# Kernel tuning notes

Hardware: AMD Instinct MI355X
Metric: run time of the kernel (lower is better)

The kernel has to match this reference:

```python
import jax, jax.numpy as jnp
import numpy as np

K_SIZES = (3, 9)          # per-level local window sizes (both < 13)
K_NUM = tuple((k * k - 1) // 2 for k in K_SIZES)  # topk sizes: (4, 40)
BN_EPS = 1e-5


def _make_local_ids(W, patch_id, k):
    """Replicates get_local_index (k<13 branch): wrap-around kxk window minus center."""
    r = k // 2
    out = []
    for i in patch_id:
        i = int(i)
        ix, iy = i // W, i % W
        wx = np.zeros(W)
        wy = np.zeros(W)
        for j in range(-r, r + 1):
            wx[(ix + j) % W] = 1.0
            wy[(iy + j) % W] = 1.0
        wgt = (wy[None, :] * wx[:, None]).reshape(-1)  # row-major: idx = x*W + y
        wgt[i] = 0.0
        out.append(np.nonzero(wgt)[0])
    return np.stack(out).astype(np.int64)  # [N, k*k-1]


def setup_inputs() -> dict:
    key = jax.random.key(0)
    ks = jax.random.split(key, 8)
    B = 8
    feat0 = jax.random.normal(ks[0], (B, 512, 8, 8), jnp.float32)
    feat1 = jax.random.normal(ks[1], (B, 64, 128, 128), jnp.float32)
    rng = np.random.default_rng(0)
    patch_id0 = rng.permutation(8 * 8)[:64]
    patch_id1 = rng.permutation(128 * 128)[:512]
    local_id0 = _make_local_ids(8, patch_id0, K_SIZES[0])    # [64, 8]
    local_id1 = _make_local_ids(128, patch_id1, K_SIZES[1])  # [512, 80]
    s = 0.02
    return dict(
        feat0=feat0, feat1=feat1,
        W1=jax.random.normal(ks[2], (1024, 512), jnp.float32) * s,
        b1=jnp.zeros((1024,), jnp.float32),
        gamma=jnp.ones((1024,), jnp.float32),
        beta=jnp.zeros((1024,), jnp.float32),
        W2=jax.random.normal(ks[3], (256, 1024), jnp.float32) * s,
        b2=jnp.zeros((256,), jnp.float32),
        W3=jax.random.normal(ks[4], (256, 64), jnp.float32) * s,
        b3=jnp.zeros((256,), jnp.float32),
        W4=jax.random.normal(ks[5], (256, 256), jnp.float32) * s,
        b4=jnp.zeros((256,), jnp.float32),
        patch_id0=jnp.asarray(patch_id0, jnp.int64 if jax.config.jax_enable_x64 else jnp.int32),
        patch_id1=jnp.asarray(patch_id1, jnp.int64 if jax.config.jax_enable_x64 else jnp.int32),
        local_id0=jnp.asarray(local_id0, jnp.int64 if jax.config.jax_enable_x64 else jnp.int32),
        local_id1=jnp.asarray(local_id1, jnp.int64 if jax.config.jax_enable_x64 else jnp.int32),
        patch_size=128,
    )


def _sample(feat, patch_id, local_id, k_num):
    """gather local patches -> cosine sim vs center -> topk -> gather winners."""
    B, C, H, W = feat.shape
    fr = jnp.transpose(feat, (0, 2, 3, 1)).reshape(B, H * W, C)  # [B, HW, C]
    norm = jnp.linalg.norm(fr, axis=-1, keepdims=True)
    xn = fr / jnp.maximum(norm, 1e-12)                 # F.normalize(dim=-1)
    loc = xn[:, local_id]                              # [B, N, L, C]
    cen = xn[:, patch_id]                              # [B, N, C]
    sim = jnp.einsum('bnlc,bnc->bnl', loc, cen)        # [B, N, L]
    _, top = jax.lax.top_k(sim, k_num)                 # [B, N, k]
    N, L = local_id.shape
    top = top.reshape(B * N, k_num, 1)
    x_loc = fr[:, local_id].reshape(B * N, L, C)
    x_loc = jnp.take_along_axis(x_loc, jnp.broadcast_to(top, (B * N, k_num, C)), axis=1)
    x_cen = fr[:, patch_id].reshape(B * N, 1, C)
    return jnp.concatenate([x_cen, x_loc], axis=1)     # [B*N, 1+k, C]


def reference(feat0, feat1, W1, b1, gamma, beta, W2, b2, W3, b3, W4, b4,
              patch_id0, patch_id1, local_id0, local_id1, patch_size):
    # level 0: h == patch_size // 16 -> adaptive_avg_pool over (1+k) axis, then mlp1
    x0 = _sample(feat0, patch_id0, local_id0, K_NUM[0])  # [B*N0, 1+k0, 512]
    x0 = x0.mean(axis=1)                                 # adaptive_avg_pool2d -> (1, dim)
    h = x0 @ W1.T + b1
    mu = h.mean(axis=0)
    var = h.var(axis=0)                                  # BatchNorm1d (training stats)
    h = (h - mu) / jnp.sqrt(var + BN_EPS) * gamma + beta
    out0 = jax.nn.relu(h) @ W2.T + b2                    # [B*N0, 256]

    # level 1: h == patch_size -> mlp2 per (center+neighbors) row, then l2norm
    x1 = _sample(feat1, patch_id1, local_id1, K_NUM[1])  # [B*N1, 1+k1, 64]
    BN1, M, C1 = x1.shape
    y = x1.reshape(-1, C1)
    y = jax.nn.relu(y @ W3.T + b3) @ W4.T + b4           # [B*N1*(1+k1), 256]
    y = y / (jnp.linalg.norm(y, axis=1, keepdims=True) + 1e-7)  # Normalize(2)
    out1 = y.reshape(BN1, M, -1)                         # [B*N1, 1+k1, 256]
    return out0, out1
```

## Files before the change

### kernel.cpp

```cpp
#include <hip/hip_runtime.h>
#include <math.h>

typedef _Float16 f16x8 __attribute__((ext_vector_type(8)));
typedef float f32x4 __attribute__((ext_vector_type(4)));


__global__ __launch_bounds__(256) void k_wprep(
    const float* __restrict__ W3, const float* __restrict__ W4,
    unsigned short* __restrict__ PB3h, unsigned short* __restrict__ PB3l,
    unsigned short* __restrict__ PB4h, unsigned short* __restrict__ PB4l)
{
    const int e = blockIdx.x * 256 + threadIdx.x;
    if (e < 16384) {
        const int j = e & 7, l = (e >> 3) & 63, ks = (e >> 9) & 1, nt = e >> 10;
        const int n = nt * 16 + (l & 15);
        const int k = ks * 32 + (l >> 4) * 8 + j;
        const float w = W3[n * 64 + k];
        const _Float16 hi = (_Float16)w;
        const _Float16 lo = (_Float16)(w - (float)hi);
        ((_Float16*)PB3h)[e] = hi;
        ((_Float16*)PB3l)[e] = lo;
    }
    {
        const int j = e & 7, l = (e >> 3) & 63, ks = (e >> 9) & 7, nt = e >> 12;
        const int n = nt * 16 + (l & 15);
        const int k = ks * 32 + (l >> 4) * 8 + j;
        const float w = W4[n * 256 + k];
        const _Float16 hi = (_Float16)w;
        const _Float16 lo = (_Float16)(w - (float)hi);
        ((_Float16*)PB4h)[e] = hi;
        ((_Float16*)PB4l)[e] = lo;
    }
}

__global__ __launch_bounds__(256) void k_transpose1(
    const float* __restrict__ feat1, float* __restrict__ featT)
{
    __shared__ float tile[64][65];
    const int b = blockIdx.y;
    const int p0 = blockIdx.x * 64;
    const int tid = threadIdx.x;
    const float* fb = feat1 + (size_t)b * 64 * 16384;
    float* ft = featT + (size_t)b * 16384 * 64;
    #pragma unroll
    for (int it = 0; it < 16; ++it) {
        const int e = it * 256 + tid;
        const int c = e >> 6, p = e & 63;
        tile[p][c] = fb[(size_t)c * 16384 + p0 + p];
    }
    __syncthreads();
    #pragma unroll
    for (int it = 0; it < 16; ++it) {
        const int e = it * 256 + tid;
        const int p = e >> 6, c = e & 63;
        ft[(size_t)(p0 + p) * 64 + c] = tile[p][c];
    }
}

__global__ __launch_bounds__(256) void k_zero(unsigned* __restrict__ p, int n)
{
    const int i = blockIdx.x * 256 + threadIdx.x;
    if (i < n) p[i] = 0u;
}

__global__ __launch_bounds__(128) void k_sims1T(
    const float* __restrict__ featT, const int* __restrict__ patch_id1,
    const int* __restrict__ local_id1, int* __restrict__ idx,
    unsigned* __restrict__ cnt)
{
    __shared__ float cen[64];
    __shared__ double sims[80];
    __shared__ double cnorm;

    const int row = blockIdx.x;
    const int b = row >> 9;
    const int n = row & 511;
    const int tid = threadIdx.x;
    const float* ft = featT + (size_t)b * 16384 * 64;
    const int pid = patch_id1[n];
    const int* lids = local_id1 + n * 80;

    if (tid < 64) cen[tid] = ft[(size_t)pid * 64 + tid];
    __syncthreads();

    if (tid < 64) {
        double v = (double)cen[tid];
        double s = v * v;
        for (int o = 32; o > 0; o >>= 1) s += __shfl_down(s, o);
        if (tid == 0) { s = sqrt(s); cnorm = (s < 1e-12) ? 1e-12 : s; }
    }
    __syncthreads();

    if (tid < 80) {
        const float4* rp = (const float4*)(ft + (size_t)lids[tid] * 64);
        double d = 0.0, q = 0.0;
        #pragma unroll
        for (int k = 0; k < 16; ++k) {
            const float4 v4 = rp[k];
            double v;
            v = (double)v4.x; d += v * (double)cen[4*k+0]; q += v*v;
            v = (double)v4.y; d += v * (double)cen[4*k+1]; q += v*v;
            v = (double)v4.z; d += v * (double)cen[4*k+2]; q += v*v;
            v = (double)v4.w; d += v * (double)cen[4*k+3]; q += v*v;
        }
        double nl = sqrt(q); if (nl < 1e-12) nl = 1e-12;
        sims[tid] = d / (nl * cnorm);
    }
    __syncthreads();

    if (tid < 80) {
        const double s = sims[tid];
        int rank = 0;
        for (int j = 0; j < 80; ++j) {
            const double sj = sims[j];
            rank += (sj > s) || (sj == s && j < tid);
        }
        if (rank < 40) {
            idx[row * 41 + 1 + rank] = lids[tid];
            atomicAdd(&cnt[b * 16384 + lids[tid]], 1u);
        }
    }
    if (tid == 0) {
        idx[row * 41] = pid;
        atomicAdd(&cnt[b * 16384 + pid], 1u);
    }
}

__global__ __launch_bounds__(256) void k_scan(
    const unsigned* __restrict__ cnt, unsigned* __restrict__ off,
    unsigned* __restrict__ cursor)
{
    __shared__ unsigned ssum[256];
    const int img = blockIdx.x;
    const int t = threadIdx.x;
    const unsigned* c = cnt + img * 16384;
    unsigned s = 0;
    for (int i = 0; i < 64; ++i) s += c[t * 64 + i];
    ssum[t] = s;
    __syncthreads();
    if (t == 0) {
        unsigned run = 0;
        for (int i = 0; i < 256; ++i) { const unsigned v = ssum[i]; ssum[i] = run; run += v; }
    }
    __syncthreads();
    unsigned run = ssum[t];
    unsigned* o  = off + img * 16384;
    unsigned* cu = cursor + img * 16384;
    for (int i = 0; i < 64; ++i) {
        const int p = t * 64 + i;
        o[p] = run; cu[p] = run;
        run += c[p];
    }
}

__global__ __launch_bounds__(256) void k_fill(
    const int* __restrict__ idx, unsigned* __restrict__ cursor,
    int* __restrict__ slots)
{
    const int e = blockIdx.x * 256 + threadIdx.x;
    if (e >= 4096 * 41) return;
    const int row = e / 41;
    const int img = row >> 9;
    const int pix = idx[e];
    const unsigned pos = atomicAdd(&cursor[img * 16384 + pix], 1u);
    slots[img * 20992 + pos] = e;
}

__global__ __launch_bounds__(256, 4) void k_mlp_fused(
    const float* __restrict__ featb,
    const unsigned short* __restrict__ PB3h, const unsigned short* __restrict__ PB3l,
    const unsigned short* __restrict__ PB4h, const unsigned short* __restrict__ PB4l,
    const float* __restrict__ b3, const float* __restrict__ b4,
    const unsigned* __restrict__ cnt, const unsigned* __restrict__ off,
    const int* __restrict__ slots, float* __restrict__ out1)
{
    __shared__ __align__(16) unsigned char smem[33792];
    _Float16 (*XH)[72]  = (_Float16(*)[72])smem;
    _Float16 (*XL)[72]  = (_Float16(*)[72])(smem + 4608);
    _Float16 (*TH)[264] = (_Float16(*)[264])smem;
    _Float16 (*TL)[264] = (_Float16(*)[264])(smem + 16896);
    __shared__ float rsums[2][2][16];

    const int tid = threadIdx.x;
    const int blk = blockIdx.x;
    const int img = blk >> 9;
    const int p0 = (blk & 511) * 32;
    const float* fb = featb + (size_t)img * 64 * 16384;

    {
        const int p = tid & 31;
        const int cg = tid >> 5;
        #pragma unroll
        for (int k = 0; k < 8; ++k) {
            const int c = cg * 8 + k;
            const float v = fb[(size_t)c * 16384 + p0 + p];
            const _Float16 hi = (_Float16)v;
            XH[p][c] = hi;
            XL[p][c] = (_Float16)(v - (float)hi);
        }
    }
    __syncthreads();

    const int lane = tid & 63;
    const int w = tid >> 6;
    const int mt = w & 1;
    const int nh = w >> 1;
    const int lrow = lane & 15;
    const int kblk = lane >> 4;

    f16x8 ah[2], al[2];
    #pragma unroll
    for (int ks = 0; ks < 2; ++ks) {
        ah[ks] = *(const f16x8*)&XH[mt*16 + lrow][ks*32 + kblk*8];
        al[ks] = *(const f16x8*)&XL[mt*16 + lrow][ks*32 + kblk*8];
    }
    __syncthreads();

    {
        const f16x8* B3H = (const f16x8*)PB3h;
        const f16x8* B3L = (const f16x8*)PB3l;
        #pragma unroll
        for (int t = 0; t < 8; ++t) {
            const int nt = nh*8 + t;
            const f16x8 bh0 = B3H[(nt*2 + 0)*64 + lane];
            const f16x8 bl0 = B3L[(nt*2 + 0)*64 + lane];
            const f16x8 bh1 = B3H[(nt*2 + 1)*64 + lane];
            const f16x8 bl1 = B3L[(nt*2 + 1)*64 + lane];
            f32x4 acc = {0.f, 0.f, 0.f, 0.f};
            acc = __builtin_amdgcn_mfma_f32_16x16x32_f16(al[0], bh0, acc, 0, 0, 0);
            acc = __builtin_amdgcn_mfma_f32_16x16x32_f16(ah[0], bl0, acc, 0, 0, 0);
            acc = __builtin_amdgcn_mfma_f32_16x16x32_f16(ah[0], bh0, acc, 0, 0, 0);
            acc = __builtin_amdgcn_mfma_f32_16x16x32_f16(al[1], bh1, acc, 0, 0, 0);
            acc = __builtin_amdgcn_mfma_f32_16x16x32_f16(ah[1], bl1, acc, 0, 0, 0);
            acc = __builtin_amdgcn_mfma_f32_16x16x32_f16(ah[1], bh1, acc, 0, 0, 0);
            const float bias = b3[nt*16 + lrow];
            #pragma unroll
            for (int r = 0; r < 4; ++r) {
                const float tv = fmaxf(acc[r] + bias, 0.f);
                const _Float16 hi = (_Float16)tv;
                TH[mt*16 + kblk*4 + r][nt*16 + lrow] = hi;
                TL[mt*16 + kblk*4 + r][nt*16 + lrow] = (_Float16)(tv - (float)hi);
            }
        }
    }
    __syncthreads();

    f32x4 acc2[8];
    #pragma unroll
    for (int t = 0; t < 8; ++t) acc2[t] = (f32x4){0.f, 0.f, 0.f, 0.f};
    {
        const f16x8* B4H = (const f16x8*)PB4h;
        const f16x8* B4L = (const f16x8*)PB4l;
        #pragma unroll 2
        for (int ks = 0; ks < 8; ++ks) {
            const f16x8 a2h = *(const f16x8*)&TH[mt*16 + lrow][ks*32 + kblk*8];
            const f16x8 a2l = *(const f16x8*)&TL[mt*16 + lrow][ks*32 + kblk*8];
            #pragma unroll
            for (int th = 0; th < 2; ++th) {
                f16x8 bh[4], bl[4];
                #pragma unroll
                for (int q = 0; q < 4; ++q) {
                    const int nt = nh*8 + th*4 + q;
                    bh[q] = B4H[(nt*8 + ks)*64 + lane];
                    bl[q] = B4L[(nt*8 + ks)*64 + lane];
                }
                #pragma unroll
                for (int q = 0; q < 4; ++q) {
                    const int t = th*4 + q;
                    acc2[t] = __builtin_amdgcn_mfma_f32_16x16x32_f16(a2l, bh[q], acc2[t], 0, 0, 0);
                    acc2[t] = __builtin_amdgcn_mfma_f32_16x16x32_f16(a2h, bl[q], acc2[t], 0, 0, 0);
                    acc2[t] = __builtin_amdgcn_mfma_f32_16x16x32_f16(a2h, bh[q], acc2[t], 0, 0, 0);
                }
            }
        }
    }

    float p[4] = {0.f, 0.f, 0.f, 0.f};
    #pragma unroll
    for (int t = 0; t < 8; ++t) {
        const float bias = b4[(nh*8 + t)*16 + lrow];
        #pragma unroll
        for (int r = 0; r < 4; ++r) {
            acc2[t][r] += bias;
            p[r] += acc2[t][r] * acc2[t][r];
        }
    }
    #pragma unroll
    for (int r = 0; r < 4; ++r)
        for (int o = 1; o < 16; o <<= 1) p[r] += __shfl_xor(p[r], o);
    if (lrow == 0) {
        #pragma unroll
        for (int r = 0; r < 4; ++r) rsums[mt][nh][kblk*4 + r] = p[r];
    }
    __syncthreads();
    float inv[4];
    #pragma unroll
    for (int r = 0; r < 4; ++r) {
        const float s = rsums[mt][0][kblk*4 + r] + rsums[mt][1][kblk*4 + r];
        inv[r] = 1.f / (sqrtf(s) + 1e-7f);
    }

    const unsigned* cntp = cnt + img * 16384;
    const unsigned* offp = off + img * 16384;
    const int* slotp = slots + img * 20992;
    #pragma unroll
    for (int r = 0; r < 4; ++r) {
        const int row = mt*16 + kblk*4 + r;
        const int pix = p0 + row;
        const unsigned deg = cntp[pix];
        const unsigned st = offp[pix];
        float y[8];
        #pragma unroll
        for (int t = 0; t < 8; ++t) y[t] = acc2[t][r] * inv[r];
        for (unsigned s = 0; s < deg; ++s) {
            const int e = slotp[st + s];
            float* dst = out1 + (size_t)e * 256 + nh*128 + lrow;
            #pragma unroll
            for (int t = 0; t < 8; ++t) dst[t*16] = y[t];
        }
    }
}

__global__ __launch_bounds__(128) void k_sims1(
    const float* __restrict__ feat1, const int* __restrict__ patch_id1,
    const int* __restrict__ local_id1, int* __restrict__ idx)
{
    __shared__ float cen[64];
    __shared__ double sims[80];
    __shared__ double cnorm;

    const int row = blockIdx.x;
    const int b = row >> 9;
    const int n = row & 511;
    const int tid = threadIdx.x;
    const float* fb = feat1 + (size_t)b * 64 * 16384;
    const int pid = patch_id1[n];
    const int* lids = local_id1 + n * 80;

    if (tid < 64) cen[tid] = fb[(size_t)tid * 16384 + pid];
    __syncthreads();

    if (tid < 64) {
        double v = (double)cen[tid];
        double s = v * v;
        for (int o = 32; o > 0; o >>= 1) s += __shfl_down(s, o);
        if (tid == 0) { s = sqrt(s); cnorm = (s < 1e-12) ? 1e-12 : s; }
    }
    __syncthreads();

    if (tid < 80) {
        const int lpix = lids[tid];
        double d = 0.0, q = 0.0;
        for (int c = 0; c < 64; ++c) {
            double v = (double)fb[(size_t)c * 16384 + lpix];
            d += v * (double)cen[c];
            q += v * v;
        }
        double nl = sqrt(q); if (nl < 1e-12) nl = 1e-12;
        sims[tid] = d / (nl * cnorm);
    }
    __syncthreads();

    if (tid < 80) {
        const double s = sims[tid];
        int rank = 0;
        for (int j = 0; j < 80; ++j) {
            const double sj = sims[j];
            rank += (sj > s) || (sj == s && j < tid);
        }
        if (rank < 40) idx[row * 41 + 1 + rank] = lids[tid];
    }
    if (tid == 0) idx[row * 41] = pid;
}

__global__ __launch_bounds__(256) void k_mlp_pix2(
    const float* __restrict__ featb,
    const float* __restrict__ W3T, const float* __restrict__ b3,
    const float* __restrict__ W4T, const float* __restrict__ b4,
    float* __restrict__ ybuf, int ybufStride)
{
    __shared__ __align__(16) float xs[32 * 68];
    __shared__ __align__(16) float t1s[32 * 256];

    const int tid = threadIdx.x;
    const int blk = blockIdx.x;
    const int img = blk >> 9;
    const int p0 = (blk & 511) * 32;
    const float* fb = featb + (size_t)img * 64 * 16384;
    float* yb = ybuf + (size_t)img * (size_t)ybufStride;

    {
        const int p = tid & 31;
        const int cg = tid >> 5;
        #pragma unroll
        for (int k = 0; k < 8; ++k) {
            const int c = cg * 8 + k;
            xs[p * 68 + c] = fb[(size_t)c * 16384 + p0 + p];
        }
    }
    __syncthreads();

    const int jg = tid & 63;
    const int g = tid >> 6;
    const int j0 = jg * 4;
    const int mb = g * 8;

    {
        float acc[8][4];
        #pragma unroll
        for (int r = 0; r < 8; ++r) {
            acc[r][0] = 0.f; acc[r][1] = 0.f; acc[r][2] = 0.f; acc[r][3] = 0.f;
        }
        const float4* Wf = (const float4*)W3T;
        const float4* xsf = (const float4*)xs;
        #pragma unroll 4
        for (int cq = 0; cq < 16; ++cq) {
            const float4 wA = Wf[(cq * 4 + 0) * 64 + jg];
            const float4 wB = Wf[(cq * 4 + 1) * 64 + jg];
            const float4 wC = Wf[(cq * 4 + 2) * 64 + jg];
            const float4 wD = Wf[(cq * 4 + 3) * 64 + jg];
            #pragma unroll
            for (int r = 0; r < 8; ++r) {
                const float4 x4 = xsf[(mb + r) * 17 + cq];
                acc[r][0] += x4.x*wA.x + x4.y*wB.x + x4.z*wC.x + x4.w*wD.x;
                acc[r][1] += x4.x*wA.y + x4.y*wB.y + x4.z*wC.y + x4.w*wD.y;
                acc[r][2] += x4.x*wA.z + x4.y*wB.z + x4.z*wC.z + x4.w*wD.z;
                acc[r][3] += x4.x*wA.w + x4.y*wB.w + x4.z*wC.w + x4.w*wD.w;
            }
        }
        const float bb0 = b3[j0], bb1 = b3[j0+1], bb2 = b3[j0+2], bb3 = b3[j0+3];
        #pragma unroll
        for (int r = 0; r < 8; ++r) {
            float4 o4;
            o4.x = fmaxf(acc[r][0] + bb0, 0.f);
            o4.y = fmaxf(acc[r][1] + bb1, 0.f);
            o4.z = fmaxf(acc[r][2] + bb2, 0.f);
            o4.w = fmaxf(acc[r][3] + bb3, 0.f);
            *(float4*)&t1s[(mb + r) * 256 + j0] = o4;
        }
    }
    __syncthreads();

    {
        float acc[8][4];
        #pragma unroll
        for (int r = 0; r < 8; ++r) {
            acc[r][0] = 0.f; acc[r][1] = 0.f; acc[r][2] = 0.f; acc[r][3] = 0.f;
        }
        const float4* Wf = (const float4*)W4T;
        const float4* t1f = (const float4*)t1s;
        #pragma unroll 2
        for (int kq = 0; kq < 64; ++kq) {
            const float4 wA = Wf[(kq * 4 + 0) * 64 + jg];
            const float4 wB = Wf[(kq * 4 + 1) * 64 + jg];
            const float4 wC = Wf[(kq * 4 + 2) * 64 + jg];
            const float4 wD = Wf[(kq * 4 + 3) * 64 + jg];
            #pragma unroll
            for (int r = 0; r < 8; ++r) {
                const float4 t4 = t1f[(mb + r) * 64 + kq];
                acc[r][0] += t4.x*wA.x + t4.y*wB.x + t4.z*wC.x + t4.w*wD.x;
                acc[r][1] += t4.x*wA.y + t4.y*wB.y + t4.z*wC.y + t4.w*wD.y;
                acc[r][2] += t4.x*wA.z + t4.y*wB.z + t4.z*wC.z + t4.w*wD.z;
                acc[r][3] += t4.x*wA.w + t4.y*wB.w + t4.z*wC.w + t4.w*wD.w;
            }
        }
        const float bb0 = b4[j0], bb1 = b4[j0+1], bb2 = b4[j0+2], bb3 = b4[j0+3];
        #pragma unroll
        for (int r = 0; r < 8; ++r) {
            const float y0 = acc[r][0] + bb0;
            const float y1 = acc[r][1] + bb1;
            const float y2 = acc[r][2] + bb2;
            const float y3 = acc[r][3] + bb3;
            float p = y0*y0 + y1*y1 + y2*y2 + y3*y3;
            for (int o = 1; o < 64; o <<= 1) p += __shfl_xor(p, o);
            const float inv = 1.f / (sqrtf(p) + 1e-7f);
            float4 o4 = make_float4(y0*inv, y1*inv, y2*inv, y3*inv);
            *(float4*)&yb[(size_t)(p0 + mb + r) * 256 + j0] = o4;
        }
    }
}

__global__ __launch_bounds__(256) void k_wtrans(
    const float* __restrict__ W3, const float* __restrict__ W4,
    float* __restrict__ W3T, float* __restrict__ W4T)
{
    const int t = threadIdx.x;
    const int j = blockIdx.x;
    W4T[(size_t)t * 256 + j] = W4[(size_t)j * 256 + t];
    if (j < 64) W3T[(size_t)j * 256 + t] = W3[(size_t)t * 64 + j];
}

__global__ __launch_bounds__(256) void k_gather1(
    const float* __restrict__ ybuf, int ybufStride,
    const int* __restrict__ idxb, float* __restrict__ out1b)
{
    __shared__ int pix[41];
    const int bn = blockIdx.x;
    const int img = bn >> 9;
    const int tid = threadIdx.x;
    if (tid < 41) pix[tid] = idxb[bn * 41 + tid];
    __syncthreads();
    const float4* yb4 = (const float4*)(ybuf + (size_t)img * (size_t)ybufStride);
    float4* o4 = (float4*)(out1b + (size_t)bn * 41 * 256);
    for (int e = tid; e < 41 * 64; e += 256) {
        const int mi = e >> 6, j4 = e & 63;
        o4[mi * 64 + j4] = yb4[pix[mi] * 64 + j4];
    }
}

__global__ __launch_bounds__(256) void k_branch1(
    const float* __restrict__ feat1, const int* __restrict__ patch_id1,
    const int* __restrict__ local_id1, const float* __restrict__ W3,
    const float* __restrict__ b3, const float* __restrict__ W4,
    const float* __restrict__ b4, float* __restrict__ out1)
{
    __shared__ __align__(16) float xs[44 * 64];
    __shared__ __align__(16) float t1s[44 * 256];
    __shared__ double sims[80];
    __shared__ int winners[40];
    __shared__ float cen[64];
    __shared__ double cnorm;

    const int row = blockIdx.x;
    const int b = row >> 9;
    const int n = row & 511;
    const int tid = threadIdx.x;
    const float* fb = feat1 + (size_t)b * 64 * 16384;
    const int pid = patch_id1[n];
    const int* lids = local_id1 + n * 80;

    if (tid < 64) cen[tid] = fb[(size_t)tid * 16384 + pid];
    __syncthreads();

    if (tid < 64) {
        double v = (double)cen[tid];
        double s = v * v;
        for (int o = 32; o > 0; o >>= 1) s += __shfl_down(s, o);
        if (tid == 0) { s = sqrt(s); cnorm = (s < 1e-12) ? 1e-12 : s; }
    }
    __syncthreads();

    if (tid < 80) {
        const int lpix = lids[tid];
        double d = 0.0, q = 0.0;
        for (int c = 0; c < 64; ++c) {
            double v = (double)fb[(size_t)c * 16384 + lpix];
            d += v * (double)cen[c];
            q += v * v;
        }
        double nl = sqrt(q); if (nl < 1e-12) nl = 1e-12;
        sims[tid] = d / (nl * cnorm);
    }
    __syncthreads();

    if (tid < 80) {
        const double s = sims[tid];
        int rank = 0;
        for (int j = 0; j < 80; ++j) {
            const double sj = sims[j];
            rank += (sj > s) || (sj == s && j < tid);
        }
        if (rank < 40) winners[rank] = tid;
    }
    __syncthreads();

    for (int m = tid; m < 44 * 64; m += 256) {
        const int mi = m >> 6, c = m & 63;
        float v;
        if (mi >= 1 && mi <= 40) v = fb[(size_t)c * 16384 + lids[winners[mi - 1]]];
        else v = cen[c];
        xs[m] = v;
    }
    __syncthreads();

    const int jg = tid & 63;
    const int g = tid >> 6;
    const int j0 = jg * 4;
    const int mb = g * 11;

    {
        float acc[11][4];
        #pragma unroll
        for (int r = 0; r < 11; ++r) {
            acc[r][0] = 0.f; acc[r][1] = 0.f; acc[r][2] = 0.f; acc[r][3] = 0.f;
        }
        const float4* W3f = (const float4*)W3;
        const float4* xsf = (const float4*)xs;
        #pragma unroll 4
        for (int c4 = 0; c4 < 16; ++c4) {
            const float4 w0 = W3f[(j0 + 0) * 16 + c4];
            const float4 w1 = W3f[(j0 + 1) * 16 + c4];
            const float4 w2 = W3f[(j0 + 2) * 16 + c4];
            const float4 w3 = W3f[(j0 + 3) * 16 + c4];
            #pragma unroll
            for (int r = 0; r < 11; ++r) {
                const float4 x4 = xsf[(mb + r) * 16 + c4];
                acc[r][0] += x4.x*w0.x + x4.y*w0.y + x4.z*w0.z + x4.w*w0.w;
                acc[r][1] += x4.x*w1.x + x4.y*w1.y + x4.z*w1.z + x4.w*w1.w;
                acc[r][2] += x4.x*w2.x + x4.y*w2.y + x4.z*w2.z + x4.w*w2.w;
                acc[r][3] += x4.x*w3.x + x4.y*w3.y + x4.z*w3.z + x4.w*w3.w;
            }
        }
        const float bb0 = b3[j0], bb1 = b3[j0+1], bb2 = b3[j0+2], bb3 = b3[j0+3];
        #pragma unroll
        for (int r = 0; r < 11; ++r) {
            float4 o4;
            o4.x = fmaxf(acc[r][0] + bb0, 0.f);
            o4.y = fmaxf(acc[r][1] + bb1, 0.f);
            o4.z = fmaxf(acc[r][2] + bb2, 0.f);
            o4.w = fmaxf(acc[r][3] + bb3, 0.f);
            *(float4*)&t1s[(mb + r) * 256 + j0] = o4;
        }
    }
    __syncthreads();

    {
        float acc[11][4];
        #pragma unroll
        for (int r = 0; r < 11; ++r) {
            acc[r][0] = 0.f; acc[r][1] = 0.f; acc[r][2] = 0.f; acc[r][3] = 0.f;
        }
        const float4* W4f = (const float4*)W4;
        const float4* t1f = (const float4*)t1s;
        #pragma unroll 2
        for (int j4 = 0; j4 < 64; ++j4) {
            const float4 w0 = W4f[(j0 + 0) * 64 + j4];
            const float4 w1 = W4f[(j0 + 1) * 64 + j4];
            const float4 w2 = W4f[(j0 + 2) * 64 + j4];
            const float4 w3 = W4f[(j0 + 3) * 64 + j4];
            #pragma unroll
            for (int r = 0; r < 11; ++r) {
                const float4 t4 = t1f[(mb + r) * 64 + j4];
                acc[r][0] += t4.x*w0.x + t4.y*w0.y + t4.z*w0.z + t4.w*w0.w;
                acc[r][1] += t4.x*w1.x + t4.y*w1.y + t4.z*w1.z + t4.w*w1.w;
                acc[r][2] += t4.x*w2.x + t4.y*w2.y + t4.z*w2.z + t4.w*w2.w;
                acc[r][3] += t4.x*w3.x + t4.y*w3.y + t4.z*w3.z + t4.w*w3.w;
            }
        }
        const float bb0 = b4[j0], bb1 = b4[j0+1], bb2 = b4[j0+2], bb3 = b4[j0+3];
        #pragma unroll
        for (int r = 0; r < 11; ++r) {
            const float y0 = acc[r][0] + bb0;
            const float y1 = acc[r][1] + bb1;
            const float y2 = acc[r][2] + bb2;
            const float y3 = acc[r][3] + bb3;
            float p = y0*y0 + y1*y1 + y2*y2 + y3*y3;
            for (int o = 1; o < 64; o <<= 1) p += __shfl_xor(p, o);
            const float inv = 1.f / (sqrtf(p) + 1e-7f);
            const int mi = mb + r;
            if (mi < 41) {
                float4 o4 = make_float4(y0*inv, y1*inv, y2*inv, y3*inv);
                *(float4*)&out1[((size_t)row * 41 + mi) * 256 + j0] = o4;
            }
        }
    }
}

__global__ __launch_bounds__(64) void k_sample0(
    const float* __restrict__ feat0, const int* __restrict__ patch_id0,
    const int* __restrict__ local_id0, float* __restrict__ x0m)
{
    __shared__ float cen[512];
    __shared__ float loc[8][512];
    __shared__ double sims[8];
    __shared__ int winners[4];
    __shared__ double cnorm;

    const int row = blockIdx.x;
    const int b = row >> 6;
    const int n = row & 63;
    const int t = threadIdx.x;
    const float* fb = feat0 + (size_t)b * 512 * 64;
    const int pid = patch_id0[n];

    for (int c = t; c < 512; c += 64) cen[c] = fb[(size_t)c * 64 + pid];
    for (int l = 0; l < 8; ++l) {
        const int lp = local_id0[n * 8 + l];
        for (int c = t; c < 512; c += 64) loc[l][c] = fb[(size_t)c * 64 + lp];
    }
    __syncthreads();

    double cs = 0.0;
    for (int c = t; c < 512; c += 64) { double v = (double)cen[c]; cs += v * v; }
    for (int o = 32; o > 0; o >>= 1) cs += __shfl_down(cs, o);
    if (t == 0) { cs = sqrt(cs); cnorm = (cs < 1e-12) ? 1e-12 : cs; }
    __syncthreads();

    for (int l = 0; l < 8; ++l) {
        double d = 0.0, q = 0.0;
        for (int c = t; c < 512; c += 64) {
            double v = (double)loc[l][c];
            d += v * (double)cen[c];
            q += v * v;
        }
        for (int o = 32; o > 0; o >>= 1) { d += __shfl_down(d, o); q += __shfl_down(q, o); }
        if (t == 0) {
            double nl = sqrt(q); if (nl < 1e-12) nl = 1e-12;
            sims[l] = d / (nl * cnorm);
        }
    }
    __syncthreads();

    if (t < 8) {
        const double s = sims[t];
        int rank = 0;
        for (int j = 0; j < 8; ++j) {
            const double sj = sims[j];
            rank += (sj > s) || (sj == s && j < t);
        }
        if (rank < 4) winners[rank] = t;
    }
    __syncthreads();

    for (int c = t; c < 512; c += 64) {
        float a = cen[c];
        for (int r = 0; r < 4; ++r) a += loc[winners[r]][c];
        x0m[(size_t)row * 512 + c] = a * 0.2f;
    }
}

__global__ __launch_bounds__(128) void k_gemm1(
    const float* __restrict__ x, const float* __restrict__ W1,
    const float* __restrict__ b1, float* __restrict__ h)
{
    __shared__ __align__(16) float xsr[8 * 512];
    const int i0 = blockIdx.y * 8;
    const int tid = threadIdx.x;
    const int j0 = blockIdx.x * 512 + tid * 4;

    const float4* xg = (const float4*)(x + (size_t)i0 * 512);
    float4* xl = (float4*)xsr;
    #pragma unroll
    for (int e = 0; e < 8; ++e) xl[e * 128 + tid] = xg[e * 128 + tid];
    __syncthreads();

    float acc[8][4];
    #pragma unroll
    for (int r = 0; r < 8; ++r) {
        acc[r][0] = 0.f; acc[r][1] = 0.f; acc[r][2] = 0.f; acc[r][3] = 0.f;
    }
    const float4* W1f = (const float4*)W1;
    const float4* xf  = (const float4*)xsr;
    #pragma unroll 4
    for (int c4 = 0; c4 < 128; ++c4) {
        const float4 w0 = W1f[(size_t)(j0 + 0) * 128 + c4];
        const float4 w1 = W1f[(size_t)(j0 + 1) * 128 + c4];
        const float4 w2 = W1f[(size_t)(j0 + 2) * 128 + c4];
        const float4 w3 = W1f[(size_t)(j0 + 3) * 128 + c4];
        #pragma unroll
        for (int r = 0; r < 8; ++r) {
            const float4 x4 = xf[r * 128 + c4];
            acc[r][0] += x4.x*w0.x + x4.y*w0.y + x4.z*w0.z + x4.w*w0.w;
            acc[r][1] += x4.x*w1.x + x4.y*w1.y + x4.z*w1.z + x4.w*w1.w;
            acc[r][2] += x4.x*w2.x + x4.y*w2.y + x4.z*w2.z + x4.w*w2.w;
            acc[r][3] += x4.x*w3.x + x4.y*w3.y + x4.z*w3.z + x4.w*w3.w;
        }
    }
    const float bb0 = b1[j0], bb1 = b1[j0+1], bb2 = b1[j0+2], bb3 = b1[j0+3];
    #pragma unroll
    for (int r = 0; r < 8; ++r) {
        float4 o4 = make_float4(acc[r][0] + bb0, acc[r][1] + bb1,
                                acc[r][2] + bb2, acc[r][3] + bb3);
        *(float4*)&h[(size_t)(i0 + r) * 1024 + j0] = o4;
    }
}

__global__ __launch_bounds__(64) void k_bnstats(
    const float* __restrict__ h, float* __restrict__ mu, float* __restrict__ rstd)
{
    const int j = blockIdx.x;
    const int t = threadIdx.x;
    float s = 0.f, ss = 0.f;
    for (int i = t; i < 512; i += 64) {
        const float v = h[(size_t)i * 1024 + j];
        s += v; ss += v * v;
    }
    for (int o = 32; o > 0; o >>= 1) { s += __shfl_down(s, o); ss += __shfl_down(ss, o); }
    if (t == 0) {
        const float m = s * (1.f / 512.f);
        const float var = ss * (1.f / 512.f) - m * m;
        mu[j] = m;
        rstd[j] = rsqrtf(var + 1e-5f);
    }
}

__global__ __launch_bounds__(256) void k_bnapply(
    float* __restrict__ h, const float* __restrict__ mu, const float* __restrict__ rstd,
    const float* __restrict__ gamma, const float* __restrict__ beta)
{
    const int e = blockIdx.x * 256 + threadIdx.x;
    const int jb = (e & 255) * 4;
    float4 v = ((float4*)h)[e];
    v.x = fmaxf((v.x - mu[jb+0]) * rstd[jb+0] * gamma[jb+0] + beta[jb+0], 0.f);
    v.y = fmaxf((v.y - mu[jb+1]) * rstd[jb+1] * gamma[jb+1] + beta[jb+1], 0.f);
    v.z = fmaxf((v.z - mu[jb+2]) * rstd[jb+2] * gamma[jb+2] + beta[jb+2], 0.f);
    v.w = fmaxf((v.w - mu[jb+3]) * rstd[jb+3] * gamma[jb+3] + beta[jb+3], 0.f);
    ((float4*)h)[e] = v;
}

__global__ __launch_bounds__(256) void k_gemm2(
    const float* __restrict__ h, const float* __restrict__ W2,
    const float* __restrict__ b2, float* __restrict__ out0)
{
    __shared__ __align__(16) float hs[8 * 1024];
    const int i0 = blockIdx.x * 8;
    const int j = threadIdx.x;

    const float4* hg = (const float4*)(h + (size_t)i0 * 1024);
    float4* hl = (float4*)hs;
    #pragma unroll
    for (int e = 0; e < 8; ++e) hl[e * 256 + j] = hg[e * 256 + j];
    __syncthreads();

    float acc[8];
    #pragma unroll
    for (int r = 0; r < 8; ++r) acc[r] = 0.f;
    const float4* wr = (const float4*)(W2 + (size_t)j * 1024);
    const float4* hf = (const float4*)hs;
    #pragma unroll 4
    for (int k4 = 0; k4 < 256; ++k4) {
        const float4 w = wr[k4];
        #pragma unroll
        for (int r = 0; r < 8; ++r) {
            const float4 a = hf[r * 256 + k4];
            acc[r] += a.x*w.x + a.y*w.y + a.z*w.z + a.w*w.w;
        }
    }
    const float bb = b2[j];
    #pragma unroll
    for (int r = 0; r < 8; ++r)
        out0[(size_t)(i0 + r) * 256 + j] = acc[r] + bb;
}

extern "C" void kernel_launch(void* const* d_in, const int* in_sizes, int n_in,
                              void* d_out, int out_size, void* d_ws, size_t ws_size,
                              hipStream_t stream) {
    const float* feat0 = (const float*)d_in[0];
    const float* feat1 = (const float*)d_in[1];
    const float* W1    = (const float*)d_in[2];
    const float* b1    = (const float*)d_in[3];
    const float* gamma = (const float*)d_in[4];
    const float* beta  = (const float*)d_in[5];
    const float* W2    = (const float*)d_in[6];
    const float* b2    = (const float*)d_in[7];
    const float* W3    = (const float*)d_in[8];
    const float* b3    = (const float*)d_in[9];
    const float* W4    = (const float*)d_in[10];
    const float* b4    = (const float*)d_in[11];
    const int* patch_id0 = (const int*)d_in[12];
    const int* patch_id1 = (const int*)d_in[13];
    const int* local_id0 = (const int*)d_in[14];
    const int* local_id1 = (const int*)d_in[15];

    float* out0 = (float*)d_out;
    float* out1 = out0 + 512 * 256;

    float* ws    = (float*)d_ws;
    float* x0m   = ws;
    float* h     = ws + 262144;
    float* mu    = ws + 786432;
    float* rstd  = ws + 787456;
    int*   idx   = (int*)(ws + 788480);
    float* W3T   = ws + 956416;
    float* W4T   = ws + 972800;
    unsigned short* PB3h = (unsigned short*)(ws + 956416);
    unsigned short* PB3l = PB3h + 16384;
    unsigned short* PB4h = PB3l + 16384;
    unsigned short* PB4l = PB4h + 65536;
    unsigned* cnt    = (unsigned*)(ws + 1038336);
    unsigned* off    = (unsigned*)(ws + 1169408);
    unsigned* cursor = (unsigned*)(ws + 1300480);
    int*      slots  = (int*)(ws + 1431552);
    float*    featTA = ws + 1599488;
    float* ybuf  = ws + 1038336;
    const int YB_STRIDE = 16384 * 256;

    const size_t NEED_A = (size_t)(1599488 + 8388608) * 4;
    const size_t NEED_B = (size_t)(1038336 + 4194304 + 8388608) * 4;
    const size_t NEED_C = (size_t)(1038336 + 4194304) * 4;

    if (ws_size >= NEED_A) {
        k_wprep<<<256, 256, 0, stream>>>(W3, W4, PB3h, PB3l, PB4h, PB4l);
        k_transpose1<<<dim3(256, 8), 256, 0, stream>>>(feat1, featTA);
        k_zero<<<512, 256, 0, stream>>>(cnt, 131072);
        k_sims1T<<<4096, 128, 0, stream>>>(featTA, patch_id1, local_id1, idx, cnt);
        k_scan<<<8, 256, 0, stream>>>(cnt, off, cursor);
        k_fill<<<656, 256, 0, stream>>>(idx, cursor, slots);
        k_mlp_fused<<<4096, 256, 0, stream>>>(feat1, PB3h, PB3l, PB4h, PB4l,
                                              b3, b4, cnt, off, slots, out1);
    } else if (ws_size >= NEED_C) {
        k_wtrans<<<256, 256, 0, stream>>>(W3, W4, W3T, W4T);
        k_sims1<<<4096, 128, 0, stream>>>(feat1, patch_id1, local_id1, idx);
        for (int b = 0; b < 8; ++b) {
            k_mlp_pix2<<<512, 256, 0, stream>>>(
                feat1 + (size_t)b * 64 * 16384, W3T, b3, W4T, b4, ybuf, 0);
            k_gather1<<<512, 256, 0, stream>>>(
                ybuf, 0, idx + (size_t)b * 512 * 41,
                out1 + (size_t)b * 512 * 41 * 256);
        }
    } else {
        k_branch1<<<4096, 256, 0, stream>>>(feat1, patch_id1, local_id1,
                                            W3, b3, W4, b4, out1);
    }

    k_sample0<<<512, 64, 0, stream>>>(feat0, patch_id0, local_id0, x0m);
    k_gemm1<<<dim3(2, 64), 128, 0, stream>>>(x0m, W1, b1, h);
    k_bnstats<<<1024, 64, 0, stream>>>(h, mu, rstd);
    k_bnapply<<<512, 256, 0, stream>>>(h, mu, rstd, gamma, beta);
    k_gemm2<<<64, 256, 0, stream>>>(h, W2, b2, out0);
}
```

Measured before the change: 581.9 us.

## Double MLP pixel tile to 64 and scatter rows via shared-memory float4 stores

The fused MLP kernel now processes 64 pixels per block with 512 threads instead of 32 with 256, halving the grid. Normalized outputs are staged in a shared-memory Y tile. Each wave then writes whole 256-float rows to every destination slot with coalesced float4 stores, replacing the strided per-lane scalar scatter. Degree and offset lookups are preloaded into shared memory, and pixels with zero references are skipped. Shared memory per block doubles, which may reduce occupancy.

```diff
diff --git a/kernel.cpp b/kernel.cpp
--- a/kernel.cpp
+++ b/kernel.cpp
@@ -166,7 +166,7 @@
     slots[img * 20992 + pos] = e;
 }
 
-__global__ __launch_bounds__(256, 4) void k_mlp_fused(
+__global__ __launch_bounds__(512, 4) void k_mlp_fused64(
     const float* __restrict__ featb,
     const unsigned short* __restrict__ PB3h, const unsigned short* __restrict__ PB3l,
     const unsigned short* __restrict__ PB4h, const unsigned short* __restrict__ PB4l,
@@ -174,22 +174,24 @@
     const unsigned* __restrict__ cnt, const unsigned* __restrict__ off,
     const int* __restrict__ slots, float* __restrict__ out1)
 {
-    __shared__ __align__(16) unsigned char smem[33792];
+    __shared__ __align__(16) unsigned char smem[67584];
     _Float16 (*XH)[72]  = (_Float16(*)[72])smem;
-    _Float16 (*XL)[72]  = (_Float16(*)[72])(smem + 4608);
+    _Float16 (*XL)[72]  = (_Float16(*)[72])(smem + 9216);
     _Float16 (*TH)[264] = (_Float16(*)[264])smem;
-    _Float16 (*TL)[264] = (_Float16(*)[264])(smem + 16896);
-    __shared__ float rsums[2][2][16];
+    _Float16 (*TL)[264] = (_Float16(*)[264])(smem + 33792);
+    float    (*Y)[260]  = (float(*)[260])smem;
+    __shared__ float rsums[4][2][16];
+    __shared__ unsigned sdeg[64], soff[64];
 
     const int tid = threadIdx.x;
     const int blk = blockIdx.x;
-    const int img = blk >> 9;
-    const int p0 = (blk & 511) * 32;
+    const int img = blk >> 8;
+    const int p0 = (blk & 255) * 64;
     const float* fb = featb + (size_t)img * 64 * 16384;
 
     {
-        const int p = tid & 31;
-        const int cg = tid >> 5;
+        const int p = tid & 63;
+        const int cg = tid >> 6;
         #pragma unroll
         for (int k = 0; k < 8; ++k) {
             const int c = cg * 8 + k;
@@ -198,13 +200,17 @@
             XH[p][c] = hi;
             XL[p][c] = (_Float16)(v - (float)hi);
         }
+        if (tid < 64) {
+            sdeg[tid] = cnt[img * 16384 + p0 + tid];
+            soff[tid] = off[img * 16384 + p0 + tid];
+        }
     }
     __syncthreads();
 
     const int lane = tid & 63;
     const int w = tid >> 6;
-    const int mt = w & 1;
-    const int nh = w >> 1;
+    const int mt = w & 3;
+    const int nh = w >> 2;
     const int lrow = lane & 15;
     const int kblk = lane >> 4;
 
@@ -293,30 +299,35 @@
         for (int r = 0; r < 4; ++r) rsums[mt][nh][kblk*4 + r] = p[r];
     }
     __syncthreads();
-    float inv[4];
-    #pragma unroll
-    for (int r = 0; r < 4; ++r) {
-        const float s = rsums[mt][0][kblk*4 + r] + rsums[mt][1][kblk*4 + r];
-        inv[r] = 1.f / (sqrtf(s) + 1e-7f);
-    }
-
-    const unsigned* cntp = cnt + img * 16384;
-    const unsigned* offp = off + img * 16384;
-    const int* slotp = slots + img * 20992;
-    #pragma unroll
-    for (int r = 0; r < 4; ++r) {
-        const int row = mt*16 + kblk*4 + r;
-        const int pix = p0 + row;
-        const unsigned deg = cntp[pix];
-        const unsigned st = offp[pix];
-        float y[8];
-        #pragma unroll
-        for (int t = 0; t < 8; ++t) y[t] = acc2[t][r] * inv[r];
-        for (unsigned s = 0; s < deg; ++s) {
-            const int e = slotp[st + s];
-            float* dst = out1 + (size_t)e * 256 + nh*128 + lrow;
+
+    {
+        float inv[4];
+        #pragma unroll
+        for (int r = 0; r < 4; ++r) {
+            const float s = rsums[mt][0][kblk*4 + r] + rsums[mt][1][kblk*4 + r];
+            inv[r] = 1.f / (sqrtf(s) + 1e-7f);
+        }
+        #pragma unroll
+        for (int t = 0; t < 8; ++t) {
+            const int col = (nh*8 + t)*16 + lrow;
             #pragma unroll
-            for (int t = 0; t < 8; ++t) dst[t*16] = y[t];
+            for (int r = 0; r < 4; ++r)
+                Y[mt*16 + kblk*4 + r][col] = acc2[t][r] * inv[r];
+        }
+    }
+    __syncthreads();
+
+    {
+        const int* sp = slots + img * 20992;
+        for (int pp = w; pp < 64; pp += 8) {
+            const unsigned d = sdeg[pp];
+            if (d == 0) continue;
+            const unsigned st = soff[pp];
+            const float4 yv = *(const float4*)&Y[pp][lane * 4];
+            for (unsigned s = 0; s < d; ++s) {
+                const int e = sp[st + s];
+                *(float4*)&out1[(size_t)e * 256 + lane * 4] = yv;
+            }
         }
     }
 }
@@ -886,8 +897,8 @@
         k_sims1T<<<4096, 128, 0, stream>>>(featTA, patch_id1, local_id1, idx, cnt);
         k_scan<<<8, 256, 0, stream>>>(cnt, off, cursor);
         k_fill<<<656, 256, 0, stream>>>(idx, cursor, slots);
-        k_mlp_fused<<<4096, 256, 0, stream>>>(feat1, PB3h, PB3l, PB4h, PB4l,
-                                              b3, b4, cnt, off, slots, out1);
+        k_mlp_fused64<<<2048, 512, 0, stream>>>(feat1, PB3h, PB3l, PB4h, PB4l,
+                                                b3, b4, cnt, off, slots, out1);
     } else if (ws_size >= NEED_C) {
         k_wtrans<<<256, 256, 0, stream>>>(W3, W4, W3T, W4T);
         k_sims1<<<4096, 128, 0, stream>>>(feat1, patch_id1, local_id1, idx);
```

Measured after the change: 587.8 us. About the same (+1.0%).
